# Kernel optimization log

Hardware: AMD Instinct MI355X
Metric: run time of the kernel (lower is better)

Reference implementation:

```python
import jax, jax.numpy as jnp
import numpy as np

B, T, S, H, M, V, L = 16, 128, 256, 512, 512, 32000, 2


def setup_inputs() -> dict:
    key = jax.random.key(0)
    ks = jax.random.split(key, 16)
    s = 0.05
    embed = jax.random.normal(ks[3], (V, H), jnp.float32) * 0.02
    embed = embed.at[0].set(0.0)  # padding_idx=0 row is zero in nn.Embedding
    return {
        'tgt': jax.random.randint(ks[0], (B, T), 0, V),
        'hidden': jax.random.normal(ks[1], (L, B, M), jnp.float32) * 0.1,
        'enc_outs': jax.random.normal(ks[2], (B, S, M), jnp.float32) * 0.1,
        'embed': embed,
        'W_ih0': jax.random.normal(ks[4], (3 * M, H), jnp.float32) * s,
        'W_hh0': jax.random.normal(ks[5], (3 * M, M), jnp.float32) * s,
        'b_ih0': jax.random.normal(ks[6], (3 * M,), jnp.float32) * s,
        'b_hh0': jax.random.normal(ks[7], (3 * M,), jnp.float32) * s,
        'W_ih1': jax.random.normal(ks[8], (3 * M, M), jnp.float32) * s,
        'W_hh1': jax.random.normal(ks[9], (3 * M, M), jnp.float32) * s,
        'b_ih1': jax.random.normal(ks[10], (3 * M,), jnp.float32) * s,
        'b_hh1': jax.random.normal(ks[11], (3 * M,), jnp.float32) * s,
        'W_out': jax.random.normal(ks[12], (V, M), jnp.float32) * s,
        'b_out': jax.random.normal(ks[13], (V,), jnp.float32) * s,
    }


def _gru_layer(x, h0, W_ih, W_hh, b_ih, b_hh):
    """PyTorch-convention GRU layer. x: [B,T,in], h0: [B,M] -> (ys [B,T,M], hT [B,M])."""
    # precompute input-side gates for all timesteps: [B,T,3M]
    xg = jnp.einsum('bti,gi->btg', x, W_ih) + b_ih

    def step(h, xg_t):
        gh = h @ W_hh.T + b_hh
        i_r, i_z, i_n = jnp.split(xg_t, 3, axis=-1)
        h_r, h_z, h_n = jnp.split(gh, 3, axis=-1)
        r = jax.nn.sigmoid(i_r + h_r)
        z = jax.nn.sigmoid(i_z + h_z)
        n = jnp.tanh(i_n + r * h_n)
        h_new = (1.0 - z) * n + z * h
        return h_new, h_new

    hT, ys = jax.lax.scan(step, h0, jnp.swapaxes(xg, 0, 1))  # scan over time
    return jnp.swapaxes(ys, 0, 1), hT


def reference(tgt, hidden, enc_outs, embed, W_ih0, W_hh0, b_ih0, b_hh0,
              W_ih1, W_hh1, b_ih1, b_hh1, W_out, b_out):
    x = embed[tgt]  # [B,T,H]
    out0, h0f = _gru_layer(x, hidden[0], W_ih0, W_hh0, b_ih0, b_hh0)
    outputs, h1f = _gru_layer(out0, hidden[1], W_ih1, W_hh1, b_ih1, b_hh1)  # [B,T,M]
    hn = jnp.stack([h0f, h1f])  # [L,B,M]
    cn = jnp.zeros_like(hn)
    # dot-product attention, batched over all timesteps (fuses the per-ts Python loop)
    scores = jnp.einsum('btm,bsm->bts', outputs, enc_outs)
    weights = jax.nn.softmax(scores, axis=-1)
    contexts = jnp.einsum('bts,bsm->btm', weights, enc_outs)
    attn_outs = outputs + contexts
    logits = jnp.einsum('btm,vm->btv', attn_outs, W_out) + b_out  # dropout p=0 -> identity
    return logits, (hn, cn)
```

## Files before the change

### kernel.cpp

```cpp
#include <hip/hip_runtime.h>
#include <hip/hip_bf16.h>
#include <math.h>

#define B_ 16
#define T_ 128
#define S_ 256
#define H_ 512
#define M_ 512
#define V_ 32000

typedef __attribute__((ext_vector_type(8))) short short8v;
typedef __attribute__((ext_vector_type(4))) float float4v;

__global__ __launch_bounds__(128) void k_gather(const int* __restrict__ tgt,
    const float* __restrict__ embed, float* __restrict__ x)
{
  const int row = blockIdx.x;
  const int v = tgt[row];
  const float4* src = (const float4*)(embed + (size_t)v * H_);
  float4* dst = (float4*)(x + (size_t)row * H_);
  dst[threadIdx.x] = src[threadIdx.x];
}

__global__ __launch_bounds__(256) void k_gemm_nt_bias(const float* __restrict__ A,
    const float* __restrict__ Bm, const float* __restrict__ bias,
    float* __restrict__ C, int N)
{
  __shared__ float As[64][33];
  __shared__ float Bs[64][33];
  const int tid = threadIdx.x;
  const int tm = tid >> 4, tn = tid & 15;
  const float* Ab = A  + (size_t)blockIdx.y * 64 * 512;
  const float* Bb = Bm + (size_t)blockIdx.x * 64 * 512;
  float acc00=0.f,acc01=0.f,acc02=0.f,acc03=0.f;
  float acc10=0.f,acc11=0.f,acc12=0.f,acc13=0.f;
  float acc20=0.f,acc21=0.f,acc22=0.f,acc23=0.f;
  float acc30=0.f,acc31=0.f,acc32=0.f,acc33=0.f;
  for (int k0 = 0; k0 < 512; k0 += 32) {
#pragma unroll
    for (int i = 0; i < 8; ++i) {
      int v = tid + i * 256;
      int row = v >> 5, col = v & 31;
      As[row][col] = Ab[(size_t)row * 512 + k0 + col];
      Bs[row][col] = Bb[(size_t)row * 512 + k0 + col];
    }
    __syncthreads();
#pragma unroll
    for (int kk = 0; kk < 32; ++kk) {
      float a0 = As[tm*4+0][kk], a1 = As[tm*4+1][kk];
      float a2 = As[tm*4+2][kk], a3 = As[tm*4+3][kk];
      float b0 = Bs[tn*4+0][kk], b1 = Bs[tn*4+1][kk];
      float b2 = Bs[tn*4+2][kk], b3 = Bs[tn*4+3][kk];
      acc00 += a0*b0; acc01 += a0*b1; acc02 += a0*b2; acc03 += a0*b3;
      acc10 += a1*b0; acc11 += a1*b1; acc12 += a1*b2; acc13 += a1*b3;
      acc20 += a2*b0; acc21 += a2*b1; acc22 += a2*b2; acc23 += a2*b3;
      acc30 += a3*b0; acc31 += a3*b1; acc32 += a3*b2; acc33 += a3*b3;
    }
    __syncthreads();
  }
  const int mbase = blockIdx.y*64 + tm*4;
  const int nbase = blockIdx.x*64 + tn*4;
  float bj0 = bias[nbase+0], bj1 = bias[nbase+1], bj2 = bias[nbase+2], bj3 = bias[nbase+3];
  float* Cr0 = C + (size_t)(mbase+0)*N + nbase;
  float* Cr1 = C + (size_t)(mbase+1)*N + nbase;
  float* Cr2 = C + (size_t)(mbase+2)*N + nbase;
  float* Cr3 = C + (size_t)(mbase+3)*N + nbase;
  Cr0[0]=acc00+bj0; Cr0[1]=acc01+bj1; Cr0[2]=acc02+bj2; Cr0[3]=acc03+bj3;
  Cr1[0]=acc10+bj0; Cr1[1]=acc11+bj1; Cr1[2]=acc12+bj2; Cr1[3]=acc13+bj3;
  Cr2[0]=acc20+bj0; Cr2[1]=acc21+bj1; Cr2[2]=acc22+bj2; Cr2[3]=acc23+bj3;
  Cr3[0]=acc30+bj0; Cr3[1]=acc31+bj1; Cr3[2]=acc32+bj2; Cr3[3]=acc33+bj3;
}

__device__ inline void bulk8_to_lds(const float* rowbase, int sc, float* dstrow)
{
  const float* p = rowbase + sc * 4;
  float4 a, b, c, d, e, f, g, h;
  asm volatile(
    "global_load_dwordx4 %0, %[p], off sc0 sc1\n\t"
    "global_load_dwordx4 %1, %[p], off offset:256 sc0 sc1\n\t"
    "global_load_dwordx4 %2, %[p], off offset:512 sc0 sc1\n\t"
    "global_load_dwordx4 %3, %[p], off offset:768 sc0 sc1\n\t"
    "global_load_dwordx4 %4, %[p], off offset:1024 sc0 sc1\n\t"
    "global_load_dwordx4 %5, %[p], off offset:1280 sc0 sc1\n\t"
    "global_load_dwordx4 %6, %[p], off offset:1536 sc0 sc1\n\t"
    "global_load_dwordx4 %7, %[p], off offset:1792 sc0 sc1\n\t"
    "s_waitcnt vmcnt(0)"
    : "=&v"(a), "=&v"(b), "=&v"(c), "=&v"(d),
      "=&v"(e), "=&v"(f), "=&v"(g), "=&v"(h)
    : [p]"v"(p)
    : "memory");
  *(float4*)&dstrow[(0*16 + sc) * 4] = a;
  *(float4*)&dstrow[(1*16 + sc) * 4] = b;
  *(float4*)&dstrow[(2*16 + sc) * 4] = c;
  *(float4*)&dstrow[(3*16 + sc) * 4] = d;
  *(float4*)&dstrow[(4*16 + sc) * 4] = e;
  *(float4*)&dstrow[(5*16 + sc) * 4] = f;
  *(float4*)&dstrow[(6*16 + sc) * 4] = g;
  *(float4*)&dstrow[(7*16 + sc) * 4] = h;
}

__global__ __launch_bounds__(256) void k_gru2(
    const float* __restrict__ xg0,
    const float* __restrict__ Whh0, const float* __restrict__ bhh0,
    const float* __restrict__ Wih1, const float* __restrict__ bih1,
    const float* __restrict__ Whh1, const float* __restrict__ bhh1,
    const float* __restrict__ hidden,
    float* __restrict__ out0, float* __restrict__ y1, float* __restrict__ hn,
    unsigned int* __restrict__ fA, unsigned int* __restrict__ fB)
{
  __shared__ float Wl[24][520];
  __shared__ float hx[2][16 * 520];
  __shared__ float ps[24][16][17];
  const int bid = blockIdx.x;
  const int lt = threadIdx.x;

  if (bid >= 192) {
    __shared__ int done;
    if (lt == 0) done = 0;
    __syncthreads();
    const unsigned int* flag = &fB[(T_ - 1) * 128 + (bid - 192)];
    float a0 = 1.0f + lt, a1 = 2.0f + lt, a2 = 3.0f, a3 = 4.0f;
    const float mb = 1.0001f, cb = 0.9999f;
    for (;;) {
#pragma unroll 16
      for (int i = 0; i < 512; ++i) {
        a0 = __builtin_fmaf(a0, mb, cb); a1 = __builtin_fmaf(a1, mb, cb);
        a2 = __builtin_fmaf(a2, mb, cb); a3 = __builtin_fmaf(a3, mb, cb);
      }
      if (lt == 0 &&
          __hip_atomic_load(flag, __ATOMIC_RELAXED, __HIP_MEMORY_SCOPE_AGENT) != 0u)
        done = 1;
      __syncthreads();
      if (done) break;
    }
    asm volatile("" :: "v"(a0), "v"(a1), "v"(a2), "v"(a3));
    return;
  }

  const bool isB = bid >= 64;
  const int wg = isB ? bid - 64 : bid;
  const int dbase = isB ? wg * 4 : wg * 8;

  for (int r = 0; r < 24; ++r) {
    const float* src;
    if (!isB) src = Whh0 + (size_t)((r >> 3) * 512 + dbase + (r & 7)) * 512;
    else if (r < 12) src = Whh1 + (size_t)((r >> 2) * 512 + dbase + (r & 3)) * 512;
    else { int rr = r - 12; src = Wih1 + (size_t)((rr >> 2) * 512 + dbase + (rr & 3)) * 512; }
    Wl[r][lt] = src[lt];
    Wl[r][lt + 256] = src[lt + 256];
  }

  const int kq = lt & 15;
  const int bq = (lt >> 4) & 3;
  const int rgrp = lt >> 6;
  const int sb = lt >> 4;
  const int sc = lt & 15;
  float* ybuf = isB ? y1 : out0;
  const float* h0g = hidden + (isB ? 8192 : 0);

  const int rb = isB ? (lt >> 2) : (lt >> 3);
  const int rdl = isB ? (lt & 3) : (lt & 7);
  const int rdg = dbase + rdl;
  const int nred = isB ? 64 : 128;
  float bhr = 0.f, bhz = 0.f, bhn = 0.f, bir = 0.f, biz = 0.f, bin_ = 0.f;
  if (lt < nred) {
    const float* bhh = isB ? bhh1 : bhh0;
    bhr = bhh[rdg]; bhz = bhh[512 + rdg]; bhn = bhh[1024 + rdg];
    if (isB) { bir = bih1[rdg]; biz = bih1[512 + rdg]; bin_ = bih1[1024 + rdg]; }
  }

  for (int t = 0; t < T_; ++t) {
    if (!isB) {
      if (t > 0 && lt < 64) {
        unsigned v;
        do {
          v = __hip_atomic_load(&fA[(t - 1) * 64 + lt], __ATOMIC_RELAXED, __HIP_MEMORY_SCOPE_AGENT);
          if (__all(v != 0u)) break;
          __builtin_amdgcn_s_sleep(1);
        } while (true);
      }
    } else {
      if (lt < 64) {
        unsigned v;
        do {
          v = __hip_atomic_load(&fA[t * 64 + lt], __ATOMIC_RELAXED, __HIP_MEMORY_SCOPE_AGENT);
          if (__all(v != 0u)) break;
          __builtin_amdgcn_s_sleep(1);
        } while (true);
      } else if (t > 0 && lt < 192) {
        unsigned v;
        do {
          v = __hip_atomic_load(&fB[(t - 1) * 128 + (lt - 64)], __ATOMIC_RELAXED, __HIP_MEMORY_SCOPE_AGENT);
          if (__all(v != 0u)) break;
          __builtin_amdgcn_s_sleep(1);
        } while (true);
      }
    }
    __syncthreads();

    if (t == 0) {
#pragma unroll
      for (int j = 0; j < 8; ++j)
        *(float4*)&hx[0][sb * 520 + (j * 16 + sc) * 4] =
            *(const float4*)(h0g + sb * 512 + (j * 16 + sc) * 4);
    } else {
      bulk8_to_lds(ybuf + (size_t)(sb * T_ + t - 1) * 512, sc, &hx[0][sb * 520]);
    }
    if (isB)
      bulk8_to_lds(out0 + (size_t)(sb * T_ + t) * 512, sc, &hx[1][sb * 520]);
    __syncthreads();

    const float* inb = (isB && rgrp >= 2) ? &hx[1][0] : &hx[0][0];
    float acc[6][4];
#pragma unroll
    for (int jr = 0; jr < 6; ++jr)
#pragma unroll
      for (int jb = 0; jb < 4; ++jb) acc[jr][jb] = 0.f;
#pragma unroll
    for (int i = 0; i < 8; ++i) {
      const int kb = kq * 4 + i * 64;
      float4 hv0 = *(const float4*)(inb + (bq * 4 + 0) * 520 + kb);
      float4 hv1 = *(const float4*)(inb + (bq * 4 + 1) * 520 + kb);
      float4 hv2 = *(const float4*)(inb + (bq * 4 + 2) * 520 + kb);
      float4 hv3 = *(const float4*)(inb + (bq * 4 + 3) * 520 + kb);
#pragma unroll
      for (int jr = 0; jr < 6; ++jr) {
        float4 wv = *(const float4*)(&Wl[rgrp * 6 + jr][kb]);
        acc[jr][0] += wv.x*hv0.x + wv.y*hv0.y + wv.z*hv0.z + wv.w*hv0.w;
        acc[jr][1] += wv.x*hv1.x + wv.y*hv1.y + wv.z*hv1.z + wv.w*hv1.w;
        acc[jr][2] += wv.x*hv2.x + wv.y*hv2.y + wv.z*hv2.z + wv.w*hv2.w;
        acc[jr][3] += wv.x*hv3.x + wv.y*hv3.y + wv.z*hv3.z + wv.w*hv3.w;
      }
    }
#pragma unroll
    for (int jr = 0; jr < 6; ++jr)
#pragma unroll
      for (int jb = 0; jb < 4; ++jb)
        ps[rgrp * 6 + jr][bq * 4 + jb][kq] = acc[jr][jb];
    __syncthreads();

    if (lt < nred) {
      float ghr, ghz, ghn, ixr, ixz, ixn;
      if (!isB) {
        float s0 = 0.f, s1 = 0.f, s2 = 0.f;
#pragma unroll
        for (int q = 0; q < 16; ++q) {
          s0 += ps[rdl][rb][q];
          s1 += ps[8 + rdl][rb][q];
          s2 += ps[16 + rdl][rb][q];
        }
        ghr = s0 + bhr; ghz = s1 + bhz; ghn = s2 + bhn;
        const float* xrow = xg0 + (size_t)(rb * T_ + t) * 1536;
        ixr = xrow[rdg]; ixz = xrow[512 + rdg]; ixn = xrow[1024 + rdg];
      } else {
        float s0=0.f,s1=0.f,s2=0.f,s3=0.f,s4=0.f,s5=0.f;
#pragma unroll
        for (int q = 0; q < 16; ++q) {
          s0 += ps[rdl][rb][q];       s1 += ps[4 + rdl][rb][q];  s2 += ps[8 + rdl][rb][q];
          s3 += ps[12 + rdl][rb][q];  s4 += ps[16 + rdl][rb][q]; s5 += ps[20 + rdl][rb][q];
        }
        ghr = s0 + bhr; ghz = s1 + bhz; ghn = s2 + bhn;
        ixr = s3 + bir; ixz = s4 + biz; ixn = s5 + bin_;
      }
      float rr = 1.f / (1.f + expf(-(ixr + ghr)));
      float zz = 1.f / (1.f + expf(-(ixz + ghz)));
      float nn = tanhf(ixn + rr * ghn);
      float hp = hx[0][rb * 520 + rdg];
      float hnew = (1.f - zz) * nn + zz * hp;
      __hip_atomic_store(&ybuf[(size_t)(rb * T_ + t) * 512 + rdg], hnew,
                         __ATOMIC_RELAXED, __HIP_MEMORY_SCOPE_AGENT);
      if (t == T_ - 1) hn[(isB ? 8192 : 0) + rb * 512 + rdg] = hnew;
    }
    __syncthreads();
    if (lt == 0) {
      if (isB)
        __hip_atomic_store(&fB[t * 128 + wg], 1u, __ATOMIC_RELAXED, __HIP_MEMORY_SCOPE_AGENT);
      else
        __hip_atomic_store(&fA[t * 64 + wg], 1u, __ATOMIC_RELAXED, __HIP_MEMORY_SCOPE_AGENT);
    }
  }
}

__global__ __launch_bounds__(256) void k_attn(const float* __restrict__ y,
    const float* __restrict__ enc, float* __restrict__ aout)
{
  __shared__ float orow[512];
  __shared__ float wbuf[256];
  __shared__ float red[8];
  const int row = blockIdx.x;
  const int b = row >> 7;
  const int lt = threadIdx.x;
  orow[lt]       = y[(size_t)row*512 + lt];
  orow[lt + 256] = y[(size_t)row*512 + lt + 256];
  __syncthreads();
  const float* er = enc + (size_t)(b*S_ + lt) * 512;
  float acc = 0.f;
  for (int k = 0; k < 512; k += 4) {
    float4 e = *(const float4*)(er + k);
    acc += orow[k]*e.x + orow[k+1]*e.y + orow[k+2]*e.z + orow[k+3]*e.w;
  }
  float m = acc;
#pragma unroll
  for (int off = 32; off > 0; off >>= 1) m = fmaxf(m, __shfl_down(m, off));
  if ((lt & 63) == 0) red[lt >> 6] = m;
  __syncthreads();
  float mx = fmaxf(fmaxf(red[0], red[1]), fmaxf(red[2], red[3]));
  float e = expf(acc - mx);
  wbuf[lt] = e;
  float s = e;
#pragma unroll
  for (int off = 32; off > 0; off >>= 1) s += __shfl_down(s, off);
  if ((lt & 63) == 0) red[4 + (lt >> 6)] = s;
  __syncthreads();
  const float inv = 1.f / (red[4] + red[5] + red[6] + red[7]);
  const int kk = lt * 2;
  float c0 = 0.f, c1 = 0.f;
  for (int s2 = 0; s2 < S_; ++s2) {
    float ws = wbuf[s2];
    float2 ev = *(const float2*)(enc + (size_t)(b*S_ + s2)*512 + kk);
    c0 += ws * ev.x; c1 += ws * ev.y;
  }
  aout[(size_t)row*512 + kk]     = orow[kk]     + c0 * inv;
  aout[(size_t)row*512 + kk + 1] = orow[kk + 1] + c1 * inv;
}

__global__ __launch_bounds__(256) void k_gemm_bf16(const float* __restrict__ A,
    const float* __restrict__ Bm, const float* __restrict__ bias,
    float* __restrict__ C)
{
  __shared__ unsigned short As[128 * 40];
  __shared__ unsigned short Bs[128 * 40];
  const int tid = threadIdx.x;
  const int nbase = blockIdx.x * 128;
  const int mbase = blockIdx.y * 128;
  const int wv = tid >> 6;
  const int l  = tid & 63;
  const int wr = wv >> 1, wc = wv & 1;
  const int r = l & 15, q = l >> 4;

  float4v acc[4][4];
#pragma unroll
  for (int mi = 0; mi < 4; ++mi)
#pragma unroll
    for (int ni = 0; ni < 4; ++ni)
      acc[mi][ni] = (float4v){0.f, 0.f, 0.f, 0.f};

  for (int k0 = 0; k0 < 512; k0 += 32) {
    __syncthreads();
#pragma unroll
    for (int h = 0; h < 2; ++h) {
      const int c = tid + h * 256;
      const int row = c >> 2, cb = c & 3;
      const float* Ag = A + (size_t)(mbase + row) * 512 + k0 + cb * 8;
      float4 f0 = *(const float4*)(Ag);
      float4 f1 = *(const float4*)(Ag + 4);
      union { short8v v; __hip_bfloat162 h2[4]; } pa;
      pa.h2[0] = __float22bfloat162_rn({f0.x, f0.y});
      pa.h2[1] = __float22bfloat162_rn({f0.z, f0.w});
      pa.h2[2] = __float22bfloat162_rn({f1.x, f1.y});
      pa.h2[3] = __float22bfloat162_rn({f1.z, f1.w});
      *(short8v*)&As[row * 40 + cb * 8] = pa.v;
      const float* Bg = Bm + (size_t)(nbase + row) * 512 + k0 + cb * 8;
      float4 g0 = *(const float4*)(Bg);
      float4 g1 = *(const float4*)(Bg + 4);
      union { short8v v; __hip_bfloat162 h2[4]; } pb;
      pb.h2[0] = __float22bfloat162_rn({g0.x, g0.y});
      pb.h2[1] = __float22bfloat162_rn({g0.z, g0.w});
      pb.h2[2] = __float22bfloat162_rn({g1.x, g1.y});
      pb.h2[3] = __float22bfloat162_rn({g1.z, g1.w});
      *(short8v*)&Bs[row * 40 + cb * 8] = pb.v;
    }
    __syncthreads();

    short8v af[4], bf[4];
#pragma unroll
    for (int mi = 0; mi < 4; ++mi)
      af[mi] = *(short8v*)&As[(wr * 64 + mi * 16 + r) * 40 + q * 8];
#pragma unroll
    for (int ni = 0; ni < 4; ++ni)
      bf[ni] = *(short8v*)&Bs[(wc * 64 + ni * 16 + r) * 40 + q * 8];
#pragma unroll
    for (int mi = 0; mi < 4; ++mi)
#pragma unroll
      for (int ni = 0; ni < 4; ++ni)
        acc[mi][ni] = __builtin_amdgcn_mfma_f32_16x16x32_bf16(af[mi], bf[ni], acc[mi][ni], 0, 0, 0);
  }

  const int mg = mbase + wr * 64;
  const int ng = nbase + wc * 64;
#pragma unroll
  for (int ni = 0; ni < 4; ++ni) {
    const int col = ng + ni * 16 + r;
    const float bj = bias[col];
#pragma unroll
    for (int mi = 0; mi < 4; ++mi) {
      const int rowb = mg + mi * 16 + q * 4;
      float4v v = acc[mi][ni];
      C[(size_t)(rowb + 0) * V_ + col] = v[0] + bj;
      C[(size_t)(rowb + 1) * V_ + col] = v[1] + bj;
      C[(size_t)(rowb + 2) * V_ + col] = v[2] + bj;
      C[(size_t)(rowb + 3) * V_ + col] = v[3] + bj;
    }
  }
}

extern "C" void kernel_launch(void* const* d_in, const int* in_sizes, int n_in,
                              void* d_out, int out_size, void* d_ws, size_t ws_size,
                              hipStream_t stream)
{
  const int*   tgt    = (const int*)  d_in[0];
  const float* hidden = (const float*)d_in[1];
  const float* enc    = (const float*)d_in[2];
  const float* embed  = (const float*)d_in[3];
  const float* W_ih0  = (const float*)d_in[4];
  const float* W_hh0  = (const float*)d_in[5];
  const float* b_ih0  = (const float*)d_in[6];
  const float* b_hh0  = (const float*)d_in[7];
  const float* W_ih1  = (const float*)d_in[8];
  const float* W_hh1  = (const float*)d_in[9];
  const float* b_ih1  = (const float*)d_in[10];
  const float* b_hh1  = (const float*)d_in[11];
  const float* W_out  = (const float*)d_in[12];
  const float* b_out  = (const float*)d_in[13];
  float* out = (float*)d_out;

  float* ws   = (float*)d_ws;
  float* xbuf = ws;
  float* xg   = ws + 1048576;
  float* out0 = xg + 3145728;
  float* y1   = out0 + 1048576;
  unsigned int* fA = (unsigned int*)(y1 + 1048576);
  unsigned int* fB = fA + T_ * 64;

  const size_t logitsN = (size_t)(B_*T_) * V_;
  float* hn = out + logitsN;
  float* cn = hn + 16384;

  hipMemsetAsync(fA, 0, (size_t)(T_ * 64 + T_ * 128) * sizeof(unsigned int), stream);
  hipMemsetAsync(cn, 0, (size_t)16384 * sizeof(float), stream);

  k_gather<<<dim3(B_*T_), dim3(128), 0, stream>>>(tgt, embed, xbuf);
  k_gemm_nt_bias<<<dim3(1536/64, (B_*T_)/64), dim3(256), 0, stream>>>(xbuf, W_ih0, b_ih0, xg, 1536);
  k_gru2<<<dim3(256), dim3(256), 0, stream>>>(xg, W_hh0, b_hh0, W_ih1, b_ih1,
                                              W_hh1, b_hh1, hidden, out0, y1, hn, fA, fB);
  k_attn<<<dim3(B_*T_), dim3(256), 0, stream>>>(y1, enc, xbuf);
  k_gemm_bf16<<<dim3(V_/128, (B_*T_)/128), dim3(256), 0, stream>>>(xbuf, W_out, b_out, out);
}
```

Before: 1.402 ms.

## Fuse attention into idle GRU blocks and keep W_out tile resident in logits GEMM

The 64 spare blocks of the persistent GRU kernel, which used to burn FMAs as heat-padding, now poll per-timestep layer-1 completion flags and compute attention plus residual for each finished timestep. This overlaps attention with the serial recurrence and removes the separate attention launch. The logits GEMM is reorganised so each block converts its 128-row W_out slice to bf16 once into a swizzled 128KB LDS buffer, then loops over all 16 M tiles. W_out is therefore no longer re-read and re-converted for every M tile, but the kernel launches only 250 blocks at one block per CU because of the large LDS footprint.

```diff
diff --git a/kernel.cpp b/kernel.cpp
--- a/kernel.cpp
+++ b/kernel.cpp
@@ -99,41 +99,91 @@
   *(float4*)&dstrow[(7*16 + sc) * 4] = h;
 }
 
+__device__ inline float4 load16_coh(const float* p)
+{
+  float4 v;
+  asm volatile(
+    "global_load_dwordx4 %0, %1, off sc0 sc1\n\t"
+    "s_waitcnt vmcnt(0)"
+    : "=v"(v) : "v"(p) : "memory");
+  return v;
+}
+
 __global__ __launch_bounds__(256) void k_gru2(
     const float* __restrict__ xg0,
     const float* __restrict__ Whh0, const float* __restrict__ bhh0,
     const float* __restrict__ Wih1, const float* __restrict__ bih1,
     const float* __restrict__ Whh1, const float* __restrict__ bhh1,
-    const float* __restrict__ hidden,
+    const float* __restrict__ hidden, const float* __restrict__ enc,
     float* __restrict__ out0, float* __restrict__ y1, float* __restrict__ hn,
+    float* __restrict__ aout,
     unsigned int* __restrict__ fA, unsigned int* __restrict__ fB)
 {
   __shared__ float Wl[24][520];
   __shared__ float hx[2][16 * 520];
   __shared__ float ps[24][16][17];
+  __shared__ float orow[520];
+  __shared__ float wbuf[256];
+  __shared__ float red[8];
   const int bid = blockIdx.x;
   const int lt = threadIdx.x;
 
   if (bid >= 192) {
-    __shared__ int done;
-    if (lt == 0) done = 0;
-    __syncthreads();
-    const unsigned int* flag = &fB[(T_ - 1) * 128 + (bid - 192)];
-    float a0 = 1.0f + lt, a1 = 2.0f + lt, a2 = 3.0f, a3 = 4.0f;
-    const float mb = 1.0001f, cb = 0.9999f;
-    for (;;) {
-#pragma unroll 16
-      for (int i = 0; i < 512; ++i) {
-        a0 = __builtin_fmaf(a0, mb, cb); a1 = __builtin_fmaf(a1, mb, cb);
-        a2 = __builtin_fmaf(a2, mb, cb); a3 = __builtin_fmaf(a3, mb, cb);
-      }
-      if (lt == 0 &&
-          __hip_atomic_load(flag, __ATOMIC_RELAXED, __HIP_MEMORY_SCOPE_AGENT) != 0u)
-        done = 1;
+    const int w = bid - 192;
+    for (int tt = w; tt < T_; tt += 64) {
+      if (lt < 128) {
+        const unsigned int* fl = &fB[tt * 128 + lt];
+        float a0 = 1.0f + lt, a1 = 2.0f + lt, a2 = 3.0f, a3 = 4.0f;
+        while (__hip_atomic_load(fl, __ATOMIC_RELAXED, __HIP_MEMORY_SCOPE_AGENT) == 0u) {
+#pragma unroll 8
+          for (int i = 0; i < 128; ++i) {
+            a0 = __builtin_fmaf(a0, 1.0001f, 0.9999f);
+            a1 = __builtin_fmaf(a1, 1.0001f, 0.9999f);
+            a2 = __builtin_fmaf(a2, 1.0001f, 0.9999f);
+            a3 = __builtin_fmaf(a3, 1.0001f, 0.9999f);
+          }
+          asm volatile("" :: "v"(a0), "v"(a1), "v"(a2), "v"(a3));
+          __builtin_amdgcn_s_sleep(4);
+        }
+      }
       __syncthreads();
-      if (done) break;
-    }
-    asm volatile("" :: "v"(a0), "v"(a1), "v"(a2), "v"(a3));
+      for (int b = 0; b < 16; ++b) {
+        const size_t row = (size_t)(b * T_ + tt);
+        if (lt < 128)
+          *(float4*)&orow[lt * 4] = load16_coh(y1 + row * 512 + lt * 4);
+        __syncthreads();
+        const float* er = enc + (size_t)(b * S_ + lt) * 512;
+        float acc = 0.f;
+        for (int k = 0; k < 512; k += 4) {
+          float4 e = *(const float4*)(er + k);
+          acc += orow[k]*e.x + orow[k+1]*e.y + orow[k+2]*e.z + orow[k+3]*e.w;
+        }
+        float m = acc;
+#pragma unroll
+        for (int off = 32; off > 0; off >>= 1) m = fmaxf(m, __shfl_down(m, off));
+        if ((lt & 63) == 0) red[lt >> 6] = m;
+        __syncthreads();
+        float mx = fmaxf(fmaxf(red[0], red[1]), fmaxf(red[2], red[3]));
+        float e = expf(acc - mx);
+        wbuf[lt] = e;
+        float s = e;
+#pragma unroll
+        for (int off = 32; off > 0; off >>= 1) s += __shfl_down(s, off);
+        if ((lt & 63) == 0) red[4 + (lt >> 6)] = s;
+        __syncthreads();
+        const float inv = 1.f / (red[4] + red[5] + red[6] + red[7]);
+        const int kk = lt * 2;
+        float c0 = 0.f, c1 = 0.f;
+        for (int s2 = 0; s2 < S_; ++s2) {
+          float ws = wbuf[s2];
+          float2 ev = *(const float2*)(enc + (size_t)(b * S_ + s2) * 512 + kk);
+          c0 += ws * ev.x; c1 += ws * ev.y;
+        }
+        aout[row * 512 + kk]     = orow[kk]     + c0 * inv;
+        aout[row * 512 + kk + 1] = orow[kk + 1] + c1 * inv;
+        __syncthreads();
+      }
+    }
     return;
   }
 
@@ -281,125 +331,101 @@
   }
 }
 
-__global__ __launch_bounds__(256) void k_attn(const float* __restrict__ y,
-    const float* __restrict__ enc, float* __restrict__ aout)
-{
-  __shared__ float orow[512];
-  __shared__ float wbuf[256];
-  __shared__ float red[8];
-  const int row = blockIdx.x;
-  const int b = row >> 7;
-  const int lt = threadIdx.x;
-  orow[lt]       = y[(size_t)row*512 + lt];
-  orow[lt + 256] = y[(size_t)row*512 + lt + 256];
-  __syncthreads();
-  const float* er = enc + (size_t)(b*S_ + lt) * 512;
-  float acc = 0.f;
-  for (int k = 0; k < 512; k += 4) {
-    float4 e = *(const float4*)(er + k);
-    acc += orow[k]*e.x + orow[k+1]*e.y + orow[k+2]*e.z + orow[k+3]*e.w;
-  }
-  float m = acc;
-#pragma unroll
-  for (int off = 32; off > 0; off >>= 1) m = fmaxf(m, __shfl_down(m, off));
-  if ((lt & 63) == 0) red[lt >> 6] = m;
-  __syncthreads();
-  float mx = fmaxf(fmaxf(red[0], red[1]), fmaxf(red[2], red[3]));
-  float e = expf(acc - mx);
-  wbuf[lt] = e;
-  float s = e;
-#pragma unroll
-  for (int off = 32; off > 0; off >>= 1) s += __shfl_down(s, off);
-  if ((lt & 63) == 0) red[4 + (lt >> 6)] = s;
-  __syncthreads();
-  const float inv = 1.f / (red[4] + red[5] + red[6] + red[7]);
-  const int kk = lt * 2;
-  float c0 = 0.f, c1 = 0.f;
-  for (int s2 = 0; s2 < S_; ++s2) {
-    float ws = wbuf[s2];
-    float2 ev = *(const float2*)(enc + (size_t)(b*S_ + s2)*512 + kk);
-    c0 += ws * ev.x; c1 += ws * ev.y;
-  }
-  aout[(size_t)row*512 + kk]     = orow[kk]     + c0 * inv;
-  aout[(size_t)row*512 + kk + 1] = orow[kk + 1] + c1 * inv;
-}
-
-__global__ __launch_bounds__(256) void k_gemm_bf16(const float* __restrict__ A,
+__global__ __launch_bounds__(256) void k_logits(const float* __restrict__ A,
     const float* __restrict__ Bm, const float* __restrict__ bias,
     float* __restrict__ C)
 {
-  __shared__ unsigned short As[128 * 40];
-  __shared__ unsigned short Bs[128 * 40];
+  __shared__ unsigned short Bs[128 * 512];
+  __shared__ unsigned short As[128 * 64];
   const int tid = threadIdx.x;
   const int nbase = blockIdx.x * 128;
-  const int mbase = blockIdx.y * 128;
   const int wv = tid >> 6;
   const int l  = tid & 63;
   const int wr = wv >> 1, wc = wv & 1;
   const int r = l & 15, q = l >> 4;
 
-  float4v acc[4][4];
-#pragma unroll
-  for (int mi = 0; mi < 4; ++mi)
-#pragma unroll
-    for (int ni = 0; ni < 4; ++ni)
-      acc[mi][ni] = (float4v){0.f, 0.f, 0.f, 0.f};
-
-  for (int k0 = 0; k0 < 512; k0 += 32) {
-    __syncthreads();
-#pragma unroll
-    for (int h = 0; h < 2; ++h) {
-      const int c = tid + h * 256;
-      const int row = c >> 2, cb = c & 3;
-      const float* Ag = A + (size_t)(mbase + row) * 512 + k0 + cb * 8;
-      float4 f0 = *(const float4*)(Ag);
-      float4 f1 = *(const float4*)(Ag + 4);
-      union { short8v v; __hip_bfloat162 h2[4]; } pa;
-      pa.h2[0] = __float22bfloat162_rn({f0.x, f0.y});
-      pa.h2[1] = __float22bfloat162_rn({f0.z, f0.w});
-      pa.h2[2] = __float22bfloat162_rn({f1.x, f1.y});
-      pa.h2[3] = __float22bfloat162_rn({f1.z, f1.w});
-      *(short8v*)&As[row * 40 + cb * 8] = pa.v;
-      const float* Bg = Bm + (size_t)(nbase + row) * 512 + k0 + cb * 8;
-      float4 g0 = *(const float4*)(Bg);
-      float4 g1 = *(const float4*)(Bg + 4);
-      union { short8v v; __hip_bfloat162 h2[4]; } pb;
-      pb.h2[0] = __float22bfloat162_rn({g0.x, g0.y});
-      pb.h2[1] = __float22bfloat162_rn({g0.z, g0.w});
-      pb.h2[2] = __float22bfloat162_rn({g1.x, g1.y});
-      pb.h2[3] = __float22bfloat162_rn({g1.z, g1.w});
-      *(short8v*)&Bs[row * 40 + cb * 8] = pb.v;
-    }
-    __syncthreads();
-
-    short8v af[4], bf[4];
+  for (int i = 0; i < 32; ++i) {
+    const int gid = tid + i * 256;
+    const int row = gid >> 6, cg = gid & 63;
+    const float* Bg = Bm + (size_t)(nbase + row) * 512 + cg * 8;
+    float4 g0 = *(const float4*)(Bg);
+    float4 g1 = *(const float4*)(Bg + 4);
+    union { short8v v; __hip_bfloat162 h2[4]; } pb;
+    pb.h2[0] = __float22bfloat162_rn({g0.x, g0.y});
+    pb.h2[1] = __float22bfloat162_rn({g0.z, g0.w});
+    pb.h2[2] = __float22bfloat162_rn({g1.x, g1.y});
+    pb.h2[3] = __float22bfloat162_rn({g1.z, g1.w});
+    const int byte = (row * 1024 + cg * 16) ^ ((row & 7) << 4);
+    *(short8v*)&Bs[byte >> 1] = pb.v;
+  }
+  __syncthreads();
+
+  for (int m = 0; m < 16; ++m) {
+    const int mbase = m * 128;
+    float4v acc[4][4];
 #pragma unroll
     for (int mi = 0; mi < 4; ++mi)
-      af[mi] = *(short8v*)&As[(wr * 64 + mi * 16 + r) * 40 + q * 8];
-#pragma unroll
-    for (int ni = 0; ni < 4; ++ni)
-      bf[ni] = *(short8v*)&Bs[(wc * 64 + ni * 16 + r) * 40 + q * 8];
-#pragma unroll
-    for (int mi = 0; mi < 4; ++mi)
 #pragma unroll
       for (int ni = 0; ni < 4; ++ni)
-        acc[mi][ni] = __builtin_amdgcn_mfma_f32_16x16x32_bf16(af[mi], bf[ni], acc[mi][ni], 0, 0, 0);
-  }
-
-  const int mg = mbase + wr * 64;
-  const int ng = nbase + wc * 64;
-#pragma unroll
-  for (int ni = 0; ni < 4; ++ni) {
-    const int col = ng + ni * 16 + r;
-    const float bj = bias[col];
-#pragma unroll
-    for (int mi = 0; mi < 4; ++mi) {
-      const int rowb = mg + mi * 16 + q * 4;
-      float4v v = acc[mi][ni];
-      C[(size_t)(rowb + 0) * V_ + col] = v[0] + bj;
-      C[(size_t)(rowb + 1) * V_ + col] = v[1] + bj;
-      C[(size_t)(rowb + 2) * V_ + col] = v[2] + bj;
-      C[(size_t)(rowb + 3) * V_ + col] = v[3] + bj;
+        acc[mi][ni] = (float4v){0.f, 0.f, 0.f, 0.f};
+
+    for (int kc = 0; kc < 8; ++kc) {
+#pragma unroll
+      for (int i = 0; i < 4; ++i) {
+        const int gid = tid + i * 256;
+        const int row = gid >> 3, cg = gid & 7;
+        const float* Ag = A + (size_t)(mbase + row) * 512 + kc * 64 + cg * 8;
+        float4 f0 = *(const float4*)(Ag);
+        float4 f1 = *(const float4*)(Ag + 4);
+        union { short8v v; __hip_bfloat162 h2[4]; } pa;
+        pa.h2[0] = __float22bfloat162_rn({f0.x, f0.y});
+        pa.h2[1] = __float22bfloat162_rn({f0.z, f0.w});
+        pa.h2[2] = __float22bfloat162_rn({f1.x, f1.y});
+        pa.h2[3] = __float22bfloat162_rn({f1.z, f1.w});
+        const int byte = (row * 128 + cg * 16) ^ ((row & 7) << 4);
+        *(short8v*)&As[byte >> 1] = pa.v;
+      }
+      __syncthreads();
+
+#pragma unroll
+      for (int k0s = 0; k0s < 2; ++k0s) {
+        short8v af[4], bf[4];
+#pragma unroll
+        for (int mi = 0; mi < 4; ++mi) {
+          const int row = wr * 64 + mi * 16 + r;
+          const int byte = (row * 128 + k0s * 64 + q * 16) ^ ((row & 7) << 4);
+          af[mi] = *(short8v*)&As[byte >> 1];
+        }
+#pragma unroll
+        for (int ni = 0; ni < 4; ++ni) {
+          const int row = wc * 64 + ni * 16 + r;
+          const int byte = (row * 1024 + kc * 128 + k0s * 64 + q * 16) ^ ((row & 7) << 4);
+          bf[ni] = *(short8v*)&Bs[byte >> 1];
+        }
+#pragma unroll
+        for (int mi = 0; mi < 4; ++mi)
+#pragma unroll
+          for (int ni = 0; ni < 4; ++ni)
+            acc[mi][ni] = __builtin_amdgcn_mfma_f32_16x16x32_bf16(af[mi], bf[ni], acc[mi][ni], 0, 0, 0);
+      }
+      __syncthreads();
+    }
+
+    const int mg = mbase + wr * 64;
+    const int ng = nbase + wc * 64;
+#pragma unroll
+    for (int ni = 0; ni < 4; ++ni) {
+      const int col = ng + ni * 16 + r;
+      const float bj = bias[col];
+#pragma unroll
+      for (int mi = 0; mi < 4; ++mi) {
+        const int rowb = mg + mi * 16 + q * 4;
+        float4v v = acc[mi][ni];
+        C[(size_t)(rowb + 0) * V_ + col] = v[0] + bj;
+        C[(size_t)(rowb + 1) * V_ + col] = v[1] + bj;
+        C[(size_t)(rowb + 2) * V_ + col] = v[2] + bj;
+        C[(size_t)(rowb + 3) * V_ + col] = v[3] + bj;
+      }
     }
   }
 }
@@ -442,7 +468,7 @@
   k_gather<<<dim3(B_*T_), dim3(128), 0, stream>>>(tgt, embed, xbuf);
   k_gemm_nt_bias<<<dim3(1536/64, (B_*T_)/64), dim3(256), 0, stream>>>(xbuf, W_ih0, b_ih0, xg, 1536);
   k_gru2<<<dim3(256), dim3(256), 0, stream>>>(xg, W_hh0, b_hh0, W_ih1, b_ih1,
-                                              W_hh1, b_hh1, hidden, out0, y1, hn, fA, fB);
-  k_attn<<<dim3(B_*T_), dim3(256), 0, stream>>>(y1, enc, xbuf);
-  k_gemm_bf16<<<dim3(V_/128, (B_*T_)/128), dim3(256), 0, stream>>>(xbuf, W_out, b_out, out);
-}
+                                              W_hh1, b_hh1, hidden, enc,
+                                              out0, y1, hn, xbuf, fA, fB);
+  k_logits<<<dim3(V_/128), dim3(256), 0, stream>>>(xbuf, W_out, b_out, out);
+}
```

Measured after the change: 1.621 ms. 15.7% more time.

## Keep full W_out tile resident in LDS and loop over all M rows per block

Applied to the files above, without the earlier changes.

The logits GEMM now launches one block per 128-column slice of the vocabulary. Each block converts its 128x512 slice of W_out to bf16 once and keeps it in LDS, then loops over all 16 row tiles of the activations. LDS accesses use an XOR swizzle to avoid bank conflicts. This removes the 16x redundant global reads and bf16 conversion of W_out. In exchange, 144KB of LDS per block leaves one block per CU and cuts the grid from 4000 to 250 blocks, so occupancy and load balance across the CUs may suffer.

```diff
diff --git a/kernel.cpp b/kernel.cpp
--- a/kernel.cpp
+++ b/kernel.cpp
@@ -324,82 +324,101 @@
   aout[(size_t)row*512 + kk + 1] = orow[kk + 1] + c1 * inv;
 }
 
-__global__ __launch_bounds__(256) void k_gemm_bf16(const float* __restrict__ A,
+__global__ __launch_bounds__(256) void k_logits(const float* __restrict__ A,
     const float* __restrict__ Bm, const float* __restrict__ bias,
     float* __restrict__ C)
 {
-  __shared__ unsigned short As[128 * 40];
-  __shared__ unsigned short Bs[128 * 40];
+  __shared__ unsigned short Bs[128 * 512];
+  __shared__ unsigned short As[128 * 64];
   const int tid = threadIdx.x;
   const int nbase = blockIdx.x * 128;
-  const int mbase = blockIdx.y * 128;
   const int wv = tid >> 6;
   const int l  = tid & 63;
   const int wr = wv >> 1, wc = wv & 1;
   const int r = l & 15, q = l >> 4;
 
-  float4v acc[4][4];
-#pragma unroll
-  for (int mi = 0; mi < 4; ++mi)
-#pragma unroll
-    for (int ni = 0; ni < 4; ++ni)
-      acc[mi][ni] = (float4v){0.f, 0.f, 0.f, 0.f};
-
-  for (int k0 = 0; k0 < 512; k0 += 32) {
-    __syncthreads();
-#pragma unroll
-    for (int h = 0; h < 2; ++h) {
-      const int c = tid + h * 256;
-      const int row = c >> 2, cb = c & 3;
-      const float* Ag = A + (size_t)(mbase + row) * 512 + k0 + cb * 8;
-      float4 f0 = *(const float4*)(Ag);
-      float4 f1 = *(const float4*)(Ag + 4);
-      union { short8v v; __hip_bfloat162 h2[4]; } pa;
-      pa.h2[0] = __float22bfloat162_rn({f0.x, f0.y});
-      pa.h2[1] = __float22bfloat162_rn({f0.z, f0.w});
-      pa.h2[2] = __float22bfloat162_rn({f1.x, f1.y});
-      pa.h2[3] = __float22bfloat162_rn({f1.z, f1.w});
-      *(short8v*)&As[row * 40 + cb * 8] = pa.v;
-      const float* Bg = Bm + (size_t)(nbase + row) * 512 + k0 + cb * 8;
-      float4 g0 = *(const float4*)(Bg);
-      float4 g1 = *(const float4*)(Bg + 4);
-      union { short8v v; __hip_bfloat162 h2[4]; } pb;
-      pb.h2[0] = __float22bfloat162_rn({g0.x, g0.y});
-      pb.h2[1] = __float22bfloat162_rn({g0.z, g0.w});
-      pb.h2[2] = __float22bfloat162_rn({g1.x, g1.y});
-      pb.h2[3] = __float22bfloat162_rn({g1.z, g1.w});
-      *(short8v*)&Bs[row * 40 + cb * 8] = pb.v;
-    }
-    __syncthreads();
-
-    short8v af[4], bf[4];
+  for (int i = 0; i < 32; ++i) {
+    const int gid = tid + i * 256;
+    const int row = gid >> 6, cg = gid & 63;
+    const float* Bg = Bm + (size_t)(nbase + row) * 512 + cg * 8;
+    float4 g0 = *(const float4*)(Bg);
+    float4 g1 = *(const float4*)(Bg + 4);
+    union { short8v v; __hip_bfloat162 h2[4]; } pb;
+    pb.h2[0] = __float22bfloat162_rn({g0.x, g0.y});
+    pb.h2[1] = __float22bfloat162_rn({g0.z, g0.w});
+    pb.h2[2] = __float22bfloat162_rn({g1.x, g1.y});
+    pb.h2[3] = __float22bfloat162_rn({g1.z, g1.w});
+    const int byte = (row * 1024 + cg * 16) ^ ((row & 7) << 4);
+    *(short8v*)&Bs[byte >> 1] = pb.v;
+  }
+  __syncthreads();
+
+  for (int m = 0; m < 16; ++m) {
+    const int mbase = m * 128;
+    float4v acc[4][4];
 #pragma unroll
     for (int mi = 0; mi < 4; ++mi)
-      af[mi] = *(short8v*)&As[(wr * 64 + mi * 16 + r) * 40 + q * 8];
-#pragma unroll
-    for (int ni = 0; ni < 4; ++ni)
-      bf[ni] = *(short8v*)&Bs[(wc * 64 + ni * 16 + r) * 40 + q * 8];
-#pragma unroll
-    for (int mi = 0; mi < 4; ++mi)
 #pragma unroll
       for (int ni = 0; ni < 4; ++ni)
-        acc[mi][ni] = __builtin_amdgcn_mfma_f32_16x16x32_bf16(af[mi], bf[ni], acc[mi][ni], 0, 0, 0);
-  }
-
-  const int mg = mbase + wr * 64;
-  const int ng = nbase + wc * 64;
-#pragma unroll
-  for (int ni = 0; ni < 4; ++ni) {
-    const int col = ng + ni * 16 + r;
-    const float bj = bias[col];
-#pragma unroll
-    for (int mi = 0; mi < 4; ++mi) {
-      const int rowb = mg + mi * 16 + q * 4;
-      float4v v = acc[mi][ni];
-      C[(size_t)(rowb + 0) * V_ + col] = v[0] + bj;
-      C[(size_t)(rowb + 1) * V_ + col] = v[1] + bj;
-      C[(size_t)(rowb + 2) * V_ + col] = v[2] + bj;
-      C[(size_t)(rowb + 3) * V_ + col] = v[3] + bj;
+        acc[mi][ni] = (float4v){0.f, 0.f, 0.f, 0.f};
+
+    for (int kc = 0; kc < 8; ++kc) {
+#pragma unroll
+      for (int i = 0; i < 4; ++i) {
+        const int gid = tid + i * 256;
+        const int row = gid >> 3, cg = gid & 7;
+        const float* Ag = A + (size_t)(mbase + row) * 512 + kc * 64 + cg * 8;
+        float4 f0 = *(const float4*)(Ag);
+        float4 f1 = *(const float4*)(Ag + 4);
+        union { short8v v; __hip_bfloat162 h2[4]; } pa;
+        pa.h2[0] = __float22bfloat162_rn({f0.x, f0.y});
+        pa.h2[1] = __float22bfloat162_rn({f0.z, f0.w});
+        pa.h2[2] = __float22bfloat162_rn({f1.x, f1.y});
+        pa.h2[3] = __float22bfloat162_rn({f1.z, f1.w});
+        const int byte = (row * 128 + cg * 16) ^ ((row & 7) << 4);
+        *(short8v*)&As[byte >> 1] = pa.v;
+      }
+      __syncthreads();
+
+#pragma unroll
+      for (int k0s = 0; k0s < 2; ++k0s) {
+        short8v af[4], bf[4];
+#pragma unroll
+        for (int mi = 0; mi < 4; ++mi) {
+          const int row = wr * 64 + mi * 16 + r;
+          const int byte = (row * 128 + k0s * 64 + q * 16) ^ ((row & 7) << 4);
+          af[mi] = *(short8v*)&As[byte >> 1];
+        }
+#pragma unroll
+        for (int ni = 0; ni < 4; ++ni) {
+          const int row = wc * 64 + ni * 16 + r;
+          const int byte = (row * 1024 + kc * 128 + k0s * 64 + q * 16) ^ ((row & 7) << 4);
+          bf[ni] = *(short8v*)&Bs[byte >> 1];
+        }
+#pragma unroll
+        for (int mi = 0; mi < 4; ++mi)
+#pragma unroll
+          for (int ni = 0; ni < 4; ++ni)
+            acc[mi][ni] = __builtin_amdgcn_mfma_f32_16x16x32_bf16(af[mi], bf[ni], acc[mi][ni], 0, 0, 0);
+      }
+      __syncthreads();
+    }
+
+    const int mg = mbase + wr * 64;
+    const int ng = nbase + wc * 64;
+#pragma unroll
+    for (int ni = 0; ni < 4; ++ni) {
+      const int col = ng + ni * 16 + r;
+      const float bj = bias[col];
+#pragma unroll
+      for (int mi = 0; mi < 4; ++mi) {
+        const int rowb = mg + mi * 16 + q * 4;
+        float4v v = acc[mi][ni];
+        C[(size_t)(rowb + 0) * V_ + col] = v[0] + bj;
+        C[(size_t)(rowb + 1) * V_ + col] = v[1] + bj;
+        C[(size_t)(rowb + 2) * V_ + col] = v[2] + bj;
+        C[(size_t)(rowb + 3) * V_ + col] = v[3] + bj;
+      }
     }
   }
 }
@@ -444,5 +463,5 @@
   k_gru2<<<dim3(256), dim3(256), 0, stream>>>(xg, W_hh0, b_hh0, W_ih1, b_ih1,
                                               W_hh1, b_hh1, hidden, out0, y1, hn, fA, fB);
   k_attn<<<dim3(B_*T_), dim3(256), 0, stream>>>(y1, enc, xbuf);
-  k_gemm_bf16<<<dim3(V_/128, (B_*T_)/128), dim3(256), 0, stream>>>(xbuf, W_out, b_out, out);
-}
+  k_logits<<<dim3(V_/128), dim3(256), 0, stream>>>(xbuf, W_out, b_out, out);
+}
```

Result: no change. 1.403 ms (+0.1%).
